# Optimization experiments

Hardware: AMD Instinct MI355X
Metric: run time of the kernel (lower is better)

## Reference

```python
import jax, jax.numpy as jnp
import numpy as np

EPS = 1e-7  # Keras K.epsilon()


def setup_inputs() -> dict:
    key = jax.random.key(0)
    k_x, k_w, k_b, k_u = jax.random.split(key, 4)
    B, T, D, A = 256, 512, 256, 50
    x = jax.random.normal(k_x, (B, T, D), dtype=jnp.float32)
    # Keras initializers.get('normal') -> stddev 0.05 RandomNormal
    W = jax.random.normal(k_w, (D, A), dtype=jnp.float32) * 0.05
    b = jax.random.normal(k_b, (A,), dtype=jnp.float32) * 0.05
    u = jax.random.normal(k_u, (A, 1), dtype=jnp.float32) * 0.05
    return {"x": x, "W": W, "b": b, "u": u}


def reference(x, W, b, u):
    # uit: [B, T, A]
    uit = jnp.tanh(jnp.einsum('btd,da->bta', x, W) + b)
    # ait: [B, T] raw scores -> exp-normalize (as in original, no max-subtract)
    ait = jnp.einsum('bta,a->bt', uit, u[:, 0])
    ait = jnp.exp(ait)
    ait = ait / (jnp.sum(ait, axis=1, keepdims=True) + EPS)
    # weighted pool over time: [B, D]
    return jnp.einsum('btd,bt->bd', x, ait)
```

## Files before the change

### kernel.cpp

```cpp
#include <hip/hip_runtime.h>
#include <hip/hip_bf16.h>
#include <math.h>

#define B_  256
#define T_  512
#define D_  256
#define A_  50
#define EPS 1e-7f
#define NW  16

typedef short  short8  __attribute__((ext_vector_type(8)));
typedef float  floatx4 __attribute__((ext_vector_type(4)));

__device__ inline unsigned short f2bf(float f) {
    unsigned int u = __float_as_uint(f);
    u = (u + 0x7fffu + ((u >> 16) & 1u)) >> 16;
    return (unsigned short)u;
}

__global__ void prep_kernel(const float* __restrict__ W,
                            const float* __restrict__ bias,
                            const float* __restrict__ u,
                            unsigned short* __restrict__ Wf,
                            float* __restrict__ bu64)
{
    int idx = blockIdx.x * 256 + threadIdx.x;
    int j  = idx & 7;
    int l  = (idx >> 3) & 63;
    int ks = (idx >> 9) & 7;
    int nt = idx >> 12;
    int n  = nt * 16 + (l & 15);
    int k  = ks * 32 + (l >> 4) * 8 + j;
    float val = (n < A_) ? W[k * A_ + n] : 0.0f;
    Wf[idx] = f2bf(val);
    if (idx < 64) {
        bu64[idx]      = (idx < A_) ? bias[idx] : 0.0f;
        bu64[64 + idx] = (idx < A_) ? u[idx]    : 0.0f;
    }
}

__device__ inline void pack_bf4(short8& av, int base, float fx, float fy,
                                float fz, float fw)
{
    union { __hip_bfloat162 h2; int i; } c0, c1;
    c0.h2 = __float22bfloat162_rn(make_float2(fx, fy));
    c1.h2 = __float22bfloat162_rn(make_float2(fz, fw));
    av[base + 0] = (short)(c0.i & 0xffff);
    av[base + 1] = (short)((unsigned)c0.i >> 16);
    av[base + 2] = (short)(c1.i & 0xffff);
    av[base + 3] = (short)((unsigned)c1.i >> 16);
}

__global__ __launch_bounds__(1024)
__attribute__((amdgpu_waves_per_eu(4, 4)))
void fused_kernel(const float* __restrict__ x,
                  const unsigned short* __restrict__ Wf,
                  const float* __restrict__ bu64,
                  float* __restrict__ out)
{
    __shared__ int4  Wl[2048];
    __shared__ float s_lds[T_];
    __shared__ float part[NW * 256];

    const int tid  = threadIdx.x;
    const int w    = tid >> 6;
    const int l    = tid & 63;
    const int c    = l & 15;
    const int quad = l >> 4;
    const int bb   = blockIdx.x;

    {
        const int4* __restrict__ wsrc = (const int4*)Wf;
        Wl[tid]        = wsrc[tid];
        Wl[tid + 1024] = wsrc[tid + 1024];
    }

    const float*  __restrict__ xb  = x + (size_t)bb * T_ * D_;
    const short8* __restrict__ wl8 = (const short8*)Wl;

    float bnc[4], unc[4];
    #pragma unroll
    for (int nt = 0; nt < 4; nt++) {
        bnc[nt] = bu64[nt * 16 + c];
        unc[nt] = bu64[64 + nt * 16 + c];
    }
    __syncthreads();

    #pragma unroll
    for (int pass = 0; pass < 2; pass++) {
        const int rowbase = pass * 256 + w * 16;
        const float4* __restrict__ xrow =
            (const float4*)(xb + (size_t)(rowbase + c) * D_);

        float4 pre[16];
        #pragma unroll
        for (int i = 0; i < 16; i++)
            pre[i] = xrow[(i >> 1) * 8 + quad * 2 + (i & 1)];

        floatx4 acc[4];
        #pragma unroll
        for (int nt = 0; nt < 4; nt++) acc[nt] = (floatx4){0.f, 0.f, 0.f, 0.f};

        #pragma unroll
        for (int ks = 0; ks < 8; ks++) {
            const float4 a0 = pre[2 * ks];
            const float4 a1 = pre[2 * ks + 1];
            short8 av;
            pack_bf4(av, 0, a0.x, a0.y, a0.z, a0.w);
            pack_bf4(av, 4, a1.x, a1.y, a1.z, a1.w);
            #pragma unroll
            for (int nt = 0; nt < 4; nt++) {
                const short8 bv = wl8[(nt * 8 + ks) * 64 + l];
                acc[nt] = __builtin_amdgcn_mfma_f32_16x16x32_bf16(av, bv, acc[nt], 0, 0, 0);
            }
        }

        #pragma unroll
        for (int r = 0; r < 4; r++) {
            float v = 0.0f;
            #pragma unroll
            for (int nt = 0; nt < 4; nt++)
                v += tanhf(acc[nt][r] + bnc[nt]) * unc[nt];
            #pragma unroll
            for (int off = 1; off < 16; off <<= 1)
                v += __shfl_xor(v, off, 16);
            if (c == 0)
                s_lds[rowbase + quad * 4 + r] = expf(v);
        }
    }
    __syncthreads();

    if (tid < 512) part[tid] = s_lds[tid];
    __syncthreads();
    for (int off = 256; off > 0; off >>= 1) {
        if (tid < off) part[tid] += part[tid + off];
        __syncthreads();
    }
    const float inv = 1.0f / (part[0] + EPS);
    __syncthreads();

    float4 acc2 = make_float4(0.f, 0.f, 0.f, 0.f);
    const int t0 = w * 32;
    #pragma unroll
    for (int i = 0; i < 32; i++) {
        const float4 xv = *(const float4*)(xb + (size_t)(t0 + i) * D_ + l * 4);
        const float sv  = s_lds[t0 + i];
        acc2.x += xv.x * sv;
        acc2.y += xv.y * sv;
        acc2.z += xv.z * sv;
        acc2.w += xv.w * sv;
    }
    acc2.x *= inv; acc2.y *= inv; acc2.z *= inv; acc2.w *= inv;

    part[w * 256 + l * 4 + 0] = acc2.x;
    part[w * 256 + l * 4 + 1] = acc2.y;
    part[w * 256 + l * 4 + 2] = acc2.z;
    part[w * 256 + l * 4 + 3] = acc2.w;
    __syncthreads();

    if (tid < 256) {
        float o = 0.0f;
        #pragma unroll
        for (int wv = 0; wv < NW; wv++) o += part[wv * 256 + tid];
        out[(size_t)bb * 256 + tid] = o;
    }
}

extern "C" void kernel_launch(void* const* d_in, const int* in_sizes, int n_in,
                              void* d_out, int out_size, void* d_ws, size_t ws_size,
                              hipStream_t stream)
{
    const float* x = (const float*)d_in[0];
    const float* W = (const float*)d_in[1];
    const float* b = (const float*)d_in[2];
    const float* u = (const float*)d_in[3];

    unsigned short* Wf  = (unsigned short*)d_ws;
    float*         bu64 = (float*)(Wf + 16384);
    float*         out  = (float*)d_out;

    prep_kernel  <<<64,  256,  0, stream>>>(W, b, u, Wf, bu64);
    fused_kernel <<<B_,  1024, 0, stream>>>(x, Wf, bu64, out);
}
```

Measured before the change: 218.5 us.

## Fuse weighted pooling into score pass, reuse register tiles, double-buffer x loads

Each wave now processes 64 consecutive time rows in four 16-row tiles, with the next tile's x loads prefetched into a second register buffer. The weighted sum over time is computed from the same registers that fed the MFMA, so the second global read of x is gone, and normalization is applied at the end. Block size drops from 1024 to 512 threads, and the serial LDS tree reduction is replaced with a wave shuffle reduction. The cost is much higher register pressure (two 16-float4 prefetch buffers plus 16 float4 accumulators) and fewer waves per block, which may reduce occupancy or cause spills.

```diff
diff --git a/kernel.cpp b/kernel.cpp
--- a/kernel.cpp
+++ b/kernel.cpp
@@ -7,7 +7,7 @@
 #define D_  256
 #define A_  50
 #define EPS 1e-7f
-#define NW  16
+#define NW  8
 
 typedef short  short8  __attribute__((ext_vector_type(8)));
 typedef float  floatx4 __attribute__((ext_vector_type(4)));
@@ -51,8 +51,8 @@
     av[base + 3] = (short)((unsigned)c1.i >> 16);
 }
 
-__global__ __launch_bounds__(1024)
-__attribute__((amdgpu_waves_per_eu(4, 4)))
+__global__ __launch_bounds__(512)
+__attribute__((amdgpu_waves_per_eu(2, 2)))
 void fused_kernel(const float* __restrict__ x,
                   const unsigned short* __restrict__ Wf,
                   const float* __restrict__ bu64,
@@ -61,6 +61,7 @@
     __shared__ int4  Wl[2048];
     __shared__ float s_lds[T_];
     __shared__ float part[NW * 256];
+    __shared__ float s_inv;
 
     const int tid  = threadIdx.x;
     const int w    = tid >> 6;
@@ -71,8 +72,9 @@
 
     {
         const int4* __restrict__ wsrc = (const int4*)Wf;
-        Wl[tid]        = wsrc[tid];
-        Wl[tid + 1024] = wsrc[tid + 1024];
+        #pragma unroll
+        for (int i = 0; i < 4; i++)
+            Wl[tid + i * 512] = wsrc[tid + i * 512];
     }
 
     const float*  __restrict__ xb  = x + (size_t)bb * T_ * D_;
@@ -86,16 +88,34 @@
     }
     __syncthreads();
 
-    #pragma unroll
-    for (int pass = 0; pass < 2; pass++) {
-        const int rowbase = pass * 256 + w * 16;
-        const float4* __restrict__ xrow =
-            (const float4*)(xb + (size_t)(rowbase + c) * D_);
-
-        float4 pre[16];
+    float4 pre[2][16];
+    float4 acc2[16];
+    #pragma unroll
+    for (int i = 0; i < 16; i++)
+        acc2[i] = make_float4(0.f, 0.f, 0.f, 0.f);
+
+    {
+        const float4* __restrict__ xr =
+            (const float4*)(xb + (size_t)(w * 64 + c) * D_);
         #pragma unroll
         for (int i = 0; i < 16; i++)
-            pre[i] = xrow[(i >> 1) * 8 + quad * 2 + (i & 1)];
+            pre[0][i] = xr[(i >> 1) * 8 + quad * 2 + (i & 1)];
+    }
+
+    #pragma unroll
+    for (int t = 0; t < 4; t++) {
+        const int cur = t & 1;
+        const int nxt = cur ^ 1;
+
+        if (t < 3) {
+            const float4* __restrict__ xr =
+                (const float4*)(xb + (size_t)(w * 64 + (t + 1) * 16 + c) * D_);
+            #pragma unroll
+            for (int i = 0; i < 16; i++)
+                pre[nxt][i] = xr[(i >> 1) * 8 + quad * 2 + (i & 1)];
+        }
+
+        const int rowbase = w * 64 + t * 16;
 
         floatx4 acc[4];
         #pragma unroll
@@ -103,8 +123,8 @@
 
         #pragma unroll
         for (int ks = 0; ks < 8; ks++) {
-            const float4 a0 = pre[2 * ks];
-            const float4 a1 = pre[2 * ks + 1];
+            const float4 a0 = pre[cur][2 * ks];
+            const float4 a1 = pre[cur][2 * ks + 1];
             short8 av;
             pack_bf4(av, 0, a0.x, a0.y, a0.z, a0.w);
             pack_bf4(av, 4, a1.x, a1.y, a1.z, a1.w);
@@ -127,42 +147,52 @@
             if (c == 0)
                 s_lds[rowbase + quad * 4 + r] = expf(v);
         }
+
+        const float ec = s_lds[rowbase + c];
+        #pragma unroll
+        for (int i = 0; i < 16; i++) {
+            acc2[i].x += pre[cur][i].x * ec;
+            acc2[i].y += pre[cur][i].y * ec;
+            acc2[i].z += pre[cur][i].z * ec;
+            acc2[i].w += pre[cur][i].w * ec;
+        }
+    }
+
+    #pragma unroll
+    for (int off = 1; off < 16; off <<= 1) {
+        #pragma unroll
+        for (int i = 0; i < 16; i++) {
+            acc2[i].x += __shfl_xor(acc2[i].x, off);
+            acc2[i].y += __shfl_xor(acc2[i].y, off);
+            acc2[i].z += __shfl_xor(acc2[i].z, off);
+            acc2[i].w += __shfl_xor(acc2[i].w, off);
+        }
+    }
+
+    if (c == 0) {
+        #pragma unroll
+        for (int i = 0; i < 16; i++) {
+            const int g = (i >> 1) * 8 + quad * 2 + (i & 1);
+            *(float4*)&part[w * 256 + g * 4] = acc2[i];
+        }
     }
     __syncthreads();
 
-    if (tid < 512) part[tid] = s_lds[tid];
-    __syncthreads();
-    for (int off = 256; off > 0; off >>= 1) {
-        if (tid < off) part[tid] += part[tid + off];
-        __syncthreads();
-    }
-    const float inv = 1.0f / (part[0] + EPS);
-    __syncthreads();
-
-    float4 acc2 = make_float4(0.f, 0.f, 0.f, 0.f);
-    const int t0 = w * 32;
-    #pragma unroll
-    for (int i = 0; i < 32; i++) {
-        const float4 xv = *(const float4*)(xb + (size_t)(t0 + i) * D_ + l * 4);
-        const float sv  = s_lds[t0 + i];
-        acc2.x += xv.x * sv;
-        acc2.y += xv.y * sv;
-        acc2.z += xv.z * sv;
-        acc2.w += xv.w * sv;
-    }
-    acc2.x *= inv; acc2.y *= inv; acc2.z *= inv; acc2.w *= inv;
-
-    part[w * 256 + l * 4 + 0] = acc2.x;
-    part[w * 256 + l * 4 + 1] = acc2.y;
-    part[w * 256 + l * 4 + 2] = acc2.z;
-    part[w * 256 + l * 4 + 3] = acc2.w;
+    if (tid < 64) {
+        float s = 0.0f;
+        #pragma unroll
+        for (int k = 0; k < 8; k++) s += s_lds[tid + k * 64];
+        #pragma unroll
+        for (int off = 1; off < 64; off <<= 1) s += __shfl_xor(s, off);
+        if (tid == 0) s_inv = 1.0f / (s + EPS);
+    }
     __syncthreads();
 
     if (tid < 256) {
         float o = 0.0f;
         #pragma unroll
         for (int wv = 0; wv < NW; wv++) o += part[wv * 256 + tid];
-        out[(size_t)bb * 256 + tid] = o;
+        out[(size_t)bb * 256 + tid] = o * s_inv;
     }
 }
 
@@ -179,6 +209,6 @@
     float*         bu64 = (float*)(Wf + 16384);
     float*         out  = (float*)d_out;
 
-    prep_kernel  <<<64,  256,  0, stream>>>(W, b, u, Wf, bu64);
-    fused_kernel <<<B_,  1024, 0, stream>>>(x, Wf, bu64, out);
-}
+    prep_kernel  <<<64,  256, 0, stream>>>(W, b, u, Wf, bu64);
+    fused_kernel <<<B_,  512, 0, stream>>>(x, Wf, bu64, out);
+}
```

New measurement: 217.7 us. Within noise of the previous version (-0.4%).

## Reuse register-held x tiles for weighted pooling via butterfly shuffle reduction

Applied to the files above, without the earlier changes.

The weighted time-pool now reuses the x values already loaded into registers for the MFMA score computation, so x is read from global memory once instead of twice. Each wave covers a contiguous 32-row slice, scales its register tiles by the exp scores, and reduces across the 16 row lanes with a select-and-shuffle butterfly that leaves each lane holding distinct columns. The tree reduction of the score sum is replaced by a single-wave shuffle reduction, and the normalisation is applied once at the output. The cost is many cross-lane shuffles and higher register pressure; the waves-per-EU attribute is relaxed to a minimum only.

```diff
diff --git a/kernel.cpp b/kernel.cpp
--- a/kernel.cpp
+++ b/kernel.cpp
@@ -51,8 +51,20 @@
     av[base + 3] = (short)((unsigned)c1.i >> 16);
 }
 
+__device__ inline float4 shflxor4(float4 v, int m) {
+    return make_float4(__shfl_xor(v.x, m), __shfl_xor(v.y, m),
+                       __shfl_xor(v.z, m), __shfl_xor(v.w, m));
+}
+__device__ inline float4 add4(float4 a, float4 b) {
+    return make_float4(a.x + b.x, a.y + b.y, a.z + b.z, a.w + b.w);
+}
+__device__ inline float4 sel4(bool p, float4 a, float4 b) {
+    return make_float4(p ? a.x : b.x, p ? a.y : b.y,
+                       p ? a.z : b.z, p ? a.w : b.w);
+}
+
 __global__ __launch_bounds__(1024)
-__attribute__((amdgpu_waves_per_eu(4, 4)))
+__attribute__((amdgpu_waves_per_eu(4)))
 void fused_kernel(const float* __restrict__ x,
                   const unsigned short* __restrict__ Wf,
                   const float* __restrict__ bu64,
@@ -61,6 +73,7 @@
     __shared__ int4  Wl[2048];
     __shared__ float s_lds[T_];
     __shared__ float part[NW * 256];
+    __shared__ float s_inv;
 
     const int tid  = threadIdx.x;
     const int w    = tid >> 6;
@@ -86,16 +99,18 @@
     }
     __syncthreads();
 
+    float4 accp = make_float4(0.f, 0.f, 0.f, 0.f);
+
     #pragma unroll
-    for (int pass = 0; pass < 2; pass++) {
-        const int rowbase = pass * 256 + w * 16;
-        const float4* __restrict__ xrow =
+    for (int t = 0; t < 2; t++) {
+        const int rowbase = w * 32 + t * 16;
+        const float4* __restrict__ xr =
             (const float4*)(xb + (size_t)(rowbase + c) * D_);
 
         float4 pre[16];
         #pragma unroll
         for (int i = 0; i < 16; i++)
-            pre[i] = xrow[(i >> 1) * 8 + quad * 2 + (i & 1)];
+            pre[i] = xr[(i >> 1) * 8 + quad * 2 + (i & 1)];
 
         floatx4 acc[4];
         #pragma unroll
@@ -127,42 +142,63 @@
             if (c == 0)
                 s_lds[rowbase + quad * 4 + r] = expf(v);
         }
-    }
+
+        const float ec = s_lds[rowbase + c];
+
+        float4 v16[16];
+        #pragma unroll
+        for (int i = 0; i < 16; i++)
+            v16[i] = make_float4(pre[i].x * ec, pre[i].y * ec,
+                                 pre[i].z * ec, pre[i].w * ec);
+
+        float4 h8[8];
+        #pragma unroll
+        for (int j = 0; j < 8; j++) {
+            const float4 a = v16[j], b = v16[j + 8];
+            h8[j] = add4(sel4((c & 8) != 0, b, a),
+                         shflxor4(sel4((c & 8) != 0, a, b), 8));
+        }
+        float4 h4[4];
+        #pragma unroll
+        for (int j = 0; j < 4; j++) {
+            const float4 a = h8[j], b = h8[j + 4];
+            h4[j] = add4(sel4((c & 4) != 0, b, a),
+                         shflxor4(sel4((c & 4) != 0, a, b), 4));
+        }
+        float4 h2[2];
+        #pragma unroll
+        for (int j = 0; j < 2; j++) {
+            const float4 a = h4[j], b = h4[j + 2];
+            h2[j] = add4(sel4((c & 2) != 0, b, a),
+                         shflxor4(sel4((c & 2) != 0, a, b), 2));
+        }
+        {
+            const float4 a = h2[0], b = h2[1];
+            const float4 h1 = add4(sel4((c & 1) != 0, b, a),
+                                   shflxor4(sel4((c & 1) != 0, a, b), 1));
+            accp = add4(accp, h1);
+        }
+    }
+
+    const int g = (c >> 1) * 8 + quad * 2 + (c & 1);
+    *(float4*)&part[w * 256 + g * 4] = accp;
     __syncthreads();
 
-    if (tid < 512) part[tid] = s_lds[tid];
-    __syncthreads();
-    for (int off = 256; off > 0; off >>= 1) {
-        if (tid < off) part[tid] += part[tid + off];
-        __syncthreads();
-    }
-    const float inv = 1.0f / (part[0] + EPS);
-    __syncthreads();
-
-    float4 acc2 = make_float4(0.f, 0.f, 0.f, 0.f);
-    const int t0 = w * 32;
-    #pragma unroll
-    for (int i = 0; i < 32; i++) {
-        const float4 xv = *(const float4*)(xb + (size_t)(t0 + i) * D_ + l * 4);
-        const float sv  = s_lds[t0 + i];
-        acc2.x += xv.x * sv;
-        acc2.y += xv.y * sv;
-        acc2.z += xv.z * sv;
-        acc2.w += xv.w * sv;
-    }
-    acc2.x *= inv; acc2.y *= inv; acc2.z *= inv; acc2.w *= inv;
-
-    part[w * 256 + l * 4 + 0] = acc2.x;
-    part[w * 256 + l * 4 + 1] = acc2.y;
-    part[w * 256 + l * 4 + 2] = acc2.z;
-    part[w * 256 + l * 4 + 3] = acc2.w;
+    if (tid < 64) {
+        float s = 0.0f;
+        #pragma unroll
+        for (int k = 0; k < 8; k++) s += s_lds[tid + k * 64];
+        #pragma unroll
+        for (int off = 1; off < 64; off <<= 1) s += __shfl_xor(s, off);
+        if (tid == 0) s_inv = 1.0f / (s + EPS);
+    }
     __syncthreads();
 
     if (tid < 256) {
         float o = 0.0f;
         #pragma unroll
         for (int wv = 0; wv < NW; wv++) o += part[wv * 256 + tid];
-        out[(size_t)bb * 256 + tid] = o;
+        out[(size_t)bb * 256 + tid] = o * s_inv;
     }
 }
 
```

New measurement: 221.8 us. About the same (+1.5%).
